# Performance work log

Measured on AMD Instinct MI355X. Metric: run time of the kernel, lower is better.

## Reference

```python
import jax, jax.numpy as jnp
import numpy as np

BATCH = 32768
NUM_CLASSES = 1024  # balanced binary hierarchy => 10 levels, 1023 internal nodes


def setup_inputs() -> dict:
    key = jax.random.key(0)
    outputs = jax.random.normal(key, (BATCH, NUM_CLASSES), dtype=jnp.float32)
    return {"outputs": outputs}


def reference(outputs) -> jnp.ndarray:
    """SoftEmbeddedDecisionRules.forward for a balanced binary hierarchy.

    For every internal node: child logit = mean of raw logits over the child's
    leaf (class) set, softmax over the node's children, then multiply each
    class's running probability by the prob of the branch containing it.
    With a balanced binary tree over C classes, level l has 2^l nodes, each
    child covering a contiguous block of C / 2^(l+1) classes, so the per-node
    Python loop of the original collapses into one reshape+mean+softmax per
    level (log2(C) fused passes total).
    """
    B, C = outputs.shape
    depth = C.bit_length() - 1  # log2(C), static
    class_probs = jnp.ones((B, C), dtype=outputs.dtype)
    for level in range(depth):
        n_nodes = 1 << level
        seg = C // (2 * n_nodes)  # classes per child subtree
        # node logits: mean of raw logits over each child's class block
        node_logits = outputs.reshape(B, n_nodes, 2, seg).mean(axis=-1)  # [B, n, 2]
        probs = jax.nn.softmax(node_logits, axis=-1)  # softmax over children
        # scatter-multiply child prob onto every class in that child's subtree
        expanded = jnp.broadcast_to(probs[..., None], (B, n_nodes, 2, seg)).reshape(B, C)
        class_probs = class_probs * expanded
    return class_probs
```

## Files before the change

kernel.cpp:

```cpp
#include <hip/hip_runtime.h>


#define C 1024

__global__ __launch_bounds__(256) void hier_softmax_kernel(
    const float* __restrict__ in, float* __restrict__ out) {
    __shared__ float heap[512];
    __shared__ float pleft[256];

    const int row = blockIdx.x;
    const int tid = threadIdx.x;

    const float4 v = ((const float4*)(in + (size_t)row * C))[tid];

    const float s2a = v.x + v.y;
    const float s2b = v.z + v.w;
    const float s4  = s2a + s2b;
    heap[256 + tid] = s4;
    __syncthreads();

    for (int cnt = 128; cnt >= 1; cnt >>= 1) {
        if (tid < cnt) {
            const int n = cnt + tid;
            const float a = heap[2 * n];
            const float b = heap[2 * n + 1];
            heap[n] = a + b;
            const float inv_seg = (float)cnt * (1.0f / 512.0f);
            pleft[n] = 1.0f / (1.0f + __expf((b - a) * inv_seg));
        }
        __syncthreads();
    }

    float common = 1.0f;
    const int leaf = 256 + tid;
#pragma unroll
    for (int s = 7; s >= 0; --s) {
        const int m = leaf >> s;
        const float p = pleft[m >> 1];
        common *= (m & 1) ? (1.0f - p) : p;
    }

    const float p9 = 1.0f / (1.0f + __expf((s2b - s2a) * 0.5f));
    const float pA = 1.0f / (1.0f + __expf(v.y - v.x));
    const float pB = 1.0f / (1.0f + __expf(v.w - v.z));

    const float cl = common * p9;
    const float cr = common * (1.0f - p9);
    float4 o;
    o.x = cl * pA;
    o.y = cl * (1.0f - pA);
    o.z = cr * pB;
    o.w = cr * (1.0f - pB);
    ((float4*)(out + (size_t)row * C))[tid] = o;
}

extern "C" void kernel_launch(void* const* d_in, const int* in_sizes, int n_in,
                              void* d_out, int out_size, void* d_ws, size_t ws_size,
                              hipStream_t stream) {
    const float* in = (const float*)d_in[0];
    float* out = (float*)d_out;
    const int B = in_sizes[0] / C;
    hier_softmax_kernel<<<B, 256, 0, stream>>>(in, out);
}
```

Before: 218.8 us.

## Replace shared-memory tree reduction with wavefront shuffle butterfly

Swaps the 8-step shared-memory heap reduction, which needed a barrier at every level, for an xor-shuffle butterfly inside each 64-lane wavefront. Each lane multiplies its own branch probabilities as it goes using its sibling's partial sum. Only the four wavefront sums go through shared memory, so a single barrier remains, and the top two levels are finished redundantly by every thread. This cuts barrier and LDS traffic, at the cost of each lane doing one sigmoid per level instead of sharing them.

After: 220.4 us. Within noise of the previous version (+0.7%).

```diff
diff --git a/kernel.cpp b/kernel.cpp
--- a/kernel.cpp
+++ b/kernel.cpp
@@ -3,49 +3,48 @@
 
 #define C 1024
 
+__device__ __forceinline__ float sigd(float d) {
+    return 1.0f / (1.0f + __expf(d));
+}
+
 __global__ __launch_bounds__(256) void hier_softmax_kernel(
     const float* __restrict__ in, float* __restrict__ out) {
-    __shared__ float heap[512];
-    __shared__ float pleft[256];
-
+    __shared__ float qsum[4];
     const int row = blockIdx.x;
     const int tid = threadIdx.x;
+    const int wave = tid >> 6;
 
     const float4 v = ((const float4*)(in + (size_t)row * C))[tid];
 
-    const float s2a = v.x + v.y;
-    const float s2b = v.z + v.w;
-    const float s4  = s2a + s2b;
-    heap[256 + tid] = s4;
+    const float pA = sigd(v.y - v.x);
+    const float pB = sigd(v.w - v.z);
+    const float s2a = v.x + v.y, s2b = v.z + v.w;
+    const float p8 = sigd((s2b - s2a) * 0.5f);
+
+    float S = s2a + s2b;
+    float common = 1.0f;
+    float inv = 0.25f;
+#pragma unroll
+    for (int m = 1; m <= 32; m <<= 1) {
+        const float sib = __shfl_xor(S, m, 64);
+        common *= sigd((sib - S) * inv);
+        S += sib;
+        inv *= 0.5f;
+    }
+    if ((tid & 63) == 0) qsum[wave] = S;
     __syncthreads();
+    const float q0 = qsum[0], q1 = qsum[1], q2 = qsum[2], q3 = qsum[3];
+    const float topL = sigd(((q2 + q3) - (q0 + q1)) * (1.0f / 512.0f));
+    const float pq01 = sigd((q1 - q0) * (1.0f / 256.0f));
+    const float pq23 = sigd((q3 - q2) * (1.0f / 256.0f));
 
-    for (int cnt = 128; cnt >= 1; cnt >>= 1) {
-        if (tid < cnt) {
-            const int n = cnt + tid;
-            const float a = heap[2 * n];
-            const float b = heap[2 * n + 1];
-            heap[n] = a + b;
-            const float inv_seg = (float)cnt * (1.0f / 512.0f);
-            pleft[n] = 1.0f / (1.0f + __expf((b - a) * inv_seg));
-        }
-        __syncthreads();
-    }
+    const float pl0 = (wave < 2) ? topL : (1.0f - topL);
+    const float pqh = (wave < 2) ? pq01 : pq23;
+    const float pl1 = (wave & 1) ? (1.0f - pqh) : pqh;
+    common *= pl0 * pl1;
 
-    float common = 1.0f;
-    const int leaf = 256 + tid;
-#pragma unroll
-    for (int s = 7; s >= 0; --s) {
-        const int m = leaf >> s;
-        const float p = pleft[m >> 1];
-        common *= (m & 1) ? (1.0f - p) : p;
-    }
-
-    const float p9 = 1.0f / (1.0f + __expf((s2b - s2a) * 0.5f));
-    const float pA = 1.0f / (1.0f + __expf(v.y - v.x));
-    const float pB = 1.0f / (1.0f + __expf(v.w - v.z));
-
-    const float cl = common * p9;
-    const float cr = common * (1.0f - p9);
+    const float cl = common * p8;
+    const float cr = common * (1.0f - p8);
     float4 o;
     o.x = cl * pA;
     o.y = cl * (1.0f - pA);
```
